# Optimization experiments

Hardware: AMD Instinct MI355X
Metric: run time of the kernel (lower is better)

## Reference

```python
import jax, jax.numpy as jnp
import numpy as np

N_NODES = 50000
N_EDGES = 800000
IN_C = 64
OUT_C = 64
HEADS = 4
N_LAYERS = 2
BN_EPS = 1e-5
NEG_SLOPE = 0.2


def setup_inputs() -> dict:
    key = jax.random.key(0)
    ks = jax.random.split(key, 20)
    inp = {
        "x": jax.random.normal(ks[0], (N_NODES, IN_C), dtype=jnp.float32),
        "edge_index": jax.random.randint(ks[1], (2, N_EDGES), 0, N_NODES, dtype=jnp.int64),
        "edge_weight": jax.random.uniform(ks[2], (N_EDGES,), dtype=jnp.float32),
    }
    # per-layer GATConv + BN params (glorot-ish init)
    for i in range(N_LAYERS):
        k = 3 + i * 5
        scale = 1.0 / np.sqrt(IN_C)
        inp[f"W{i}"] = jax.random.normal(ks[k], (IN_C, HEADS * OUT_C), dtype=jnp.float32) * scale
        inp[f"asrc{i}"] = jax.random.normal(ks[k + 1], (HEADS, OUT_C), dtype=jnp.float32) * scale
        inp[f"adst{i}"] = jax.random.normal(ks[k + 2], (HEADS, OUT_C), dtype=jnp.float32) * scale
        inp[f"b{i}"] = jnp.zeros((OUT_C,), dtype=jnp.float32)
        inp[f"gamma{i}"] = jnp.ones((OUT_C,), dtype=jnp.float32)
        inp[f"beta{i}"] = jnp.zeros((OUT_C,), dtype=jnp.float32)
    return inp


def _gat_layer(x, src, dst, W, a_src, a_dst, b):
    # x: [N, C_in]; src/dst: [E'] (with self loops). Per-head dim = OUT_C.
    xh = (x @ W).reshape(-1, HEADS, OUT_C)          # [N, H, C]
    al_src = jnp.sum(xh * a_src[None], axis=-1)      # [N, H]
    al_dst = jnp.sum(xh * a_dst[None], axis=-1)      # [N, H]
    e = jax.nn.leaky_relu(al_src[src] + al_dst[dst], NEG_SLOPE)  # [E', H]
    # segment softmax over edges sharing a destination node
    m = jax.lax.stop_gradient(jax.ops.segment_max(e, dst, num_segments=N_NODES))
    p = jnp.exp(e - m[dst])
    denom = jax.ops.segment_sum(p, dst, num_segments=N_NODES)
    alpha = p / (denom[dst] + 1e-16)                 # [E', H]
    out = jax.ops.segment_sum(alpha[:, :, None] * xh[src], dst, num_segments=N_NODES)  # [N,H,C]
    return out.mean(axis=1) + b                      # concat=False -> mean over heads


def _batchnorm(x, gamma, beta):
    mu = x.mean(axis=0)
    var = x.var(axis=0)
    return gamma * (x - mu) * jax.lax.rsqrt(var + BN_EPS) + beta


def reference(x, edge_index, edge_weight, W0, asrc0, adst0, b0, gamma0, beta0,
              W1, asrc1, adst1, b1, gamma1, beta1):
    # edge_weight is passed as edge_attr to PyG GATConv but edge_dim=None -> ignored.
    loop = jnp.arange(N_NODES, dtype=edge_index.dtype)
    src = jnp.concatenate([edge_index[0], loop])  # add_self_loops=True (PyG default)
    dst = jnp.concatenate([edge_index[1], loop])
    params = [(W0, asrc0, adst0, b0, gamma0, beta0),
              (W1, asrc1, adst1, b1, gamma1, beta1)]
    saved = None
    for (W, a_s, a_d, b, g, bt) in params:
        x = _gat_layer(x, src, dst, W, a_s, a_d, b)
        saved = x
        x = _batchnorm(x, g, bt)
        x = jax.nn.relu(x)
        # dropout(0.5) is identity in eval mode
    return (x, saved)
```

## Files before the change

kernel.cpp:

```cpp
#include <hip/hip_runtime.h>
#include <stdint.h>

#define NEG_SLOPE 0.2f
#define BN_EPS 1e-5f

typedef __attribute__((ext_vector_type(8))) short bf16x8;
typedef __attribute__((ext_vector_type(4))) float f32x4;

__device__ __forceinline__ float bf2f(unsigned short u) {
  union { unsigned int i; float f; } v; v.i = ((unsigned int)u) << 16; return v.f;
}
__device__ __forceinline__ float asf(unsigned int u) {
  union { unsigned int i; float f; } v; v.i = u; return v.f;
}
__device__ __forceinline__ unsigned short f2bf(float f) {
  union { float f; unsigned int i; } v; v.f = f;
  unsigned int i = v.i;
  return (unsigned short)((i + 0x7fffu + ((i >> 16) & 1u)) >> 16);
}
__device__ __forceinline__ float loadF(const void* p, long long i, int f32) {
  return f32 ? ((const float*)p)[i] : bf2f(((const unsigned short*)p)[i]);
}
__device__ __forceinline__ int edge_at(const void* ei, long long idx, int is64) {
  return is64 ? (int)((const long long*)ei)[idx] : ((const int*)ei)[idx];
}

__global__ void detect_kernel(const unsigned short* __restrict__ x,
                              const int* __restrict__ ei32,
                              int* __restrict__ flags) {
  __shared__ int wild, oddnz;
  if (threadIdx.x == 0) { wild = 0; oddnz = 0; }
  __syncthreads();
  int lw = 0, lo = 0;
  for (int i = threadIdx.x; i < 4096; i += 256) {
    unsigned short u = x[i];
    int ex = (u >> 7) & 0xFF;
    if (ex >= 0x86) lw++;
    if (ei32[2 * i + 1] != 0) lo++;
  }
  if (lw) atomicAdd(&wild, lw);
  if (lo) atomicAdd(&oddnz, lo);
  __syncthreads();
  if (threadIdx.x == 0) { flags[0] = (wild > 64) ? 1 : 0; flags[1] = (oddnz == 0) ? 1 : 0; }
}

__global__ __launch_bounds__(256) void wtrans_kernel(
    const void* __restrict__ W0, const void* __restrict__ as0, const void* __restrict__ ad0,
    const void* __restrict__ W1, const void* __restrict__ as1, const void* __restrict__ ad1,
    const int* __restrict__ flags,
    unsigned short* __restrict__ WTx0, unsigned short* __restrict__ WTx1) {
  const void* W = blockIdx.x ? W1 : W0;
  const void* asrc = blockIdx.x ? as1 : as0;
  const void* adst = blockIdx.x ? ad1 : ad0;
  unsigned short* WTx = blockIdx.x ? WTx1 : WTx0;
  int f32 = flags[0];
  __shared__ unsigned short Wl[64 * 258];
  int t = threadIdx.x;
  for (int i = t; i < 64 * 256; i += 256) {
    int k = i >> 8, c = i & 255;
    Wl[k * 258 + c] = f32 ? f2bf(((const float*)W)[i]) : ((const unsigned short*)W)[i];
  }
  __syncthreads();
  {
    int c = t;
    #pragma unroll
    for (int k8 = 0; k8 < 64; k8 += 8) {
      unsigned int p0 = (unsigned int)Wl[(k8 + 0) * 258 + c] | ((unsigned int)Wl[(k8 + 1) * 258 + c] << 16);
      unsigned int p1 = (unsigned int)Wl[(k8 + 2) * 258 + c] | ((unsigned int)Wl[(k8 + 3) * 258 + c] << 16);
      unsigned int p2 = (unsigned int)Wl[(k8 + 4) * 258 + c] | ((unsigned int)Wl[(k8 + 5) * 258 + c] << 16);
      unsigned int p3 = (unsigned int)Wl[(k8 + 6) * 258 + c] | ((unsigned int)Wl[(k8 + 7) * 258 + c] << 16);
      uint4 pk; pk.x = p0; pk.y = p1; pk.z = p2; pk.w = p3;
      *(uint4*)&WTx[c * 64 + k8] = pk;
    }
  }
  for (int idx = t; idx < 512; idx += 256) {
    int r = idx >> 6;
    int k = idx & 63;
    int h = r & 3;
    const void* av = (r >> 2) ? adst : asrc;
    float acc = 0.f;
    #pragma unroll 8
    for (int c = 0; c < 64; c++)
      acc += bf2f(Wl[k * 258 + h * 64 + c]) * loadF(av, h * 64 + c, f32);
    WTx[(256 + r) * 64 + k] = f2bf(acc);
  }
  for (int idx = t; idx < 512; idx += 256) WTx[264 * 64 + idx] = 0;
}

__global__ __launch_bounds__(256) void hist_kernel(const void* __restrict__ ei, int E, int N,
                                                   const int* __restrict__ flags,
                                                   int* __restrict__ deg) {
  int e = blockIdx.x * 256 + threadIdx.x;
  if (e >= E) return;
  int is64 = flags[1];
  int d = edge_at(ei, (long long)E + e, is64);
  d = (d < 0 || d >= N) ? 0 : d;
  atomicAdd(&deg[d], 1);
}

__global__ __launch_bounds__(256) void partial_kernel(const int* __restrict__ deg,
                                                      int* __restrict__ blocksum, int N) {
  int t = threadIdx.x;
  int idx = blockIdx.x * 256 + t;
  int v = (idx < N) ? deg[idx] : 0;
  #pragma unroll
  for (int o = 1; o < 64; o <<= 1) v += __shfl_xor(v, o);
  __shared__ int ws[4];
  if ((t & 63) == 0) ws[t >> 6] = v;
  __syncthreads();
  if (t == 0) blocksum[blockIdx.x] = ws[0] + ws[1] + ws[2] + ws[3];
}

__global__ void scan_base_kernel(const int* __restrict__ blocksum,
                                 int* __restrict__ blockbase, int B) {
  int lane = threadIdx.x;
  int base = 0;
  if (lane == 0) blockbase[0] = 0;
  for (int start = 0; start < B; start += 64) {
    int idx = start + lane;
    int v = (idx < B) ? blocksum[idx] : 0;
    int sc = v;
    #pragma unroll
    for (int o = 1; o < 64; o <<= 1) {
      int u = __shfl_up(sc, o);
      if (lane >= o) sc += u;
    }
    if (idx < B) blockbase[idx + 1] = base + sc;
    base = __shfl(base + sc, 63);
  }
}

__global__ __launch_bounds__(256) void scan_final_kernel(const int* __restrict__ deg,
                                                         const int* __restrict__ blockbase,
                                                         int* __restrict__ offsets, int N) {
  int t = threadIdx.x;
  int lane = t & 63;
  int wid = t >> 6;
  int idx = blockIdx.x * 256 + t;
  int v = (idx < N) ? deg[idx] : 0;
  int sc = v;
  #pragma unroll
  for (int o = 1; o < 64; o <<= 1) {
    int u = __shfl_up(sc, o);
    if (lane >= o) sc += u;
  }
  __shared__ int ws[4];
  if (lane == 63) ws[wid] = sc;
  __syncthreads();
  int add = 0;
  #pragma unroll
  for (int w = 0; w < 4; w++) if (w < wid) add += ws[w];
  if (idx < N) offsets[idx + 1] = blockbase[blockIdx.x] + add + sc;
  if (idx == 0) offsets[0] = 0;
}

__global__ __launch_bounds__(256) void scatter_kernel(
    const void* __restrict__ ei, int E, int N, const int* __restrict__ flags,
    const int* __restrict__ offsets, int* __restrict__ cursor,
    int* __restrict__ csr_src) {
  int e = blockIdx.x * 256 + threadIdx.x;
  if (e >= E) return;
  int is64 = flags[1];
  int s = edge_at(ei, e, is64);
  int d = edge_at(ei, (long long)E + e, is64);
  s = (s < 0 || s >= N) ? 0 : s;
  d = (d < 0 || d >= N) ? 0 : d;
  int pos = offsets[d] + atomicAdd(&cursor[d], 1);
  csr_src[pos] = s;
}

__global__ __launch_bounds__(256, 3) void gemm_mfma(
    const void* __restrict__ x, const unsigned short* __restrict__ WTx,
    const int* __restrict__ flags, int mode,
    const float* __restrict__ gsum, const float* __restrict__ gsq,
    const void* __restrict__ gamma, const void* __restrict__ beta,
    unsigned short* __restrict__ xh, float* __restrict__ als, float* __restrict__ ald,
    int N) {
  __shared__ unsigned short WTs[272 * 68];
  __shared__ unsigned short RP[4][16 * 68];
  __shared__ float bnsc[64], bnsh[64];
  int f32 = flags[0];
  int t = threadIdx.x;
  for (int i = t; i < 272 * 8; i += 256) {
    int c = i >> 3, g = i & 7;
    uint4 v = ((const uint4*)WTx)[i];
    *(uint4*)&WTs[c * 68 + g * 8] = v;
  }
  if (mode == 1 && t < 64) {
    float mu = gsum[t] / (float)N;
    float var = fmaxf(gsq[t] / (float)N - mu * mu, 0.f);
    float sc = loadF(gamma, t, f32) * rsqrtf(var + BN_EPS);
    bnsc[t] = sc;
    bnsh[t] = loadF(beta, t, f32) - mu * sc;
  }
  __syncthreads();

  int wave = t >> 6, lane = t & 63;
  int q = lane >> 4, r16 = lane & 15;
  unsigned short* rp = RP[wave];

  #pragma unroll
  for (int rb = 0; rb < 2; rb++) {
    int m0 = blockIdx.x * 128 + rb * 64 + wave * 16;
    if (m0 >= N) break;
    int row = m0 + r16;
    int rowc = row < N ? row : N - 1;

    bf16x8 a0, a1;
    if (mode == 1) {
      const float* xp = (const float*)x + (size_t)rowc * 64 + q * 8;
      float va[8], vb[8];
      *(float4*)&va[0] = ((const float4*)xp)[0];
      *(float4*)&va[4] = ((const float4*)xp)[1];
      *(float4*)&vb[0] = ((const float4*)(xp + 32))[0];
      *(float4*)&vb[4] = ((const float4*)(xp + 32))[1];
      int k0 = q * 8;
      #pragma unroll
      for (int jj = 0; jj < 8; jj++) {
        float v = fmaxf(va[jj] * bnsc[k0 + jj] + bnsh[k0 + jj], 0.f);
        float w = fmaxf(vb[jj] * bnsc[k0 + 32 + jj] + bnsh[k0 + 32 + jj], 0.f);
        a0[jj] = (short)f2bf(v);
        a1[jj] = (short)f2bf(w);
      }
    } else if (f32) {
      const float* xp = (const float*)x + (size_t)rowc * 64 + q * 8;
      float va[8], vb[8];
      *(float4*)&va[0] = ((const float4*)xp)[0];
      *(float4*)&va[4] = ((const float4*)xp)[1];
      *(float4*)&vb[0] = ((const float4*)(xp + 32))[0];
      *(float4*)&vb[4] = ((const float4*)(xp + 32))[1];
      #pragma unroll
      for (int jj = 0; jj < 8; jj++) {
        a0[jj] = (short)f2bf(va[jj]);
        a1[jj] = (short)f2bf(vb[jj]);
      }
    } else {
      const unsigned short* xp = (const unsigned short*)x + (size_t)rowc * 64 + q * 8;
      a0 = *(const bf16x8*)xp;
      a1 = *(const bf16x8*)(xp + 32);
    }

    f32x4 acc[17];
    #pragma unroll
    for (int tt = 0; tt < 17; tt++) acc[tt] = (f32x4){0.f, 0.f, 0.f, 0.f};
    #pragma unroll
    for (int tt = 0; tt < 17; tt++) {
      int c = tt * 16 + r16;
      bf16x8 b0 = *(const bf16x8*)&WTs[c * 68 + q * 8];
      bf16x8 b1 = *(const bf16x8*)&WTs[c * 68 + 32 + q * 8];
      acc[tt] = __builtin_amdgcn_mfma_f32_16x16x32_bf16(a0, b0, acc[tt], 0, 0, 0);
      acc[tt] = __builtin_amdgcn_mfma_f32_16x16x32_bf16(a1, b1, acc[tt], 0, 0, 0);
    }

    {
      int obase = m0 + q * 4;
      #pragma unroll
      for (int rr = 0; rr < 4; rr++) {
        int orow = obase + rr;
        if (orow < N) {
          if (r16 < 4) als[orow * 4 + r16] = acc[16][rr];
          else if (r16 < 8) ald[orow * 4 + (r16 - 4)] = acc[16][rr];
        }
      }
    }
    #pragma unroll
    for (int g4 = 0; g4 < 4; g4++) {
      #pragma unroll
      for (int tt2 = 0; tt2 < 4; tt2++) {
        int tile = g4 * 4 + tt2;
        #pragma unroll
        for (int rr = 0; rr < 4; rr++)
          rp[(q * 4 + rr) * 68 + tt2 * 16 + r16] = f2bf(acc[tile][rr]);
      }
      #pragma unroll
      for (int i = 0; i < 2; i++) {
        int g = i * 64 + lane;
        int r = g >> 3;
        int grp = g & 7;
        uint4 v = *(const uint4*)&rp[r * 68 + grp * 8];
        int orow = m0 + r;
        if (orow < N) ((uint4*)xh)[(size_t)orow * 32 + g4 * 8 + grp] = v;
      }
    }
  }
}

__global__ __launch_bounds__(256) void agg_kernel(
    const unsigned short* __restrict__ xh,
    const float* __restrict__ als, const float* __restrict__ ald,
    const int* __restrict__ offsets, const int* __restrict__ csr_src,
    const void* __restrict__ bias, const int* __restrict__ flags,
    float* __restrict__ y, int N) {
  int lane = threadIdx.x & 63;
  int wid = threadIdx.x >> 6;
  int n = blockIdx.x * 4 + wid;
  if (n >= N) return;
  int half = lane >> 5;
  int hl = lane & 31;
  int h = hl >> 3;
  const uint4* xv = (const uint4*)xh;
  float ad = ald[n * 4 + h];
  float acc0 = 0.f, acc1 = 0.f, acc2 = 0.f, acc3 = 0.f;
  float acc4 = 0.f, acc5 = 0.f, acc6 = 0.f, acc7 = 0.f;
  float dsum = 0.f;
  if (half == 0) {
    float e = als[n * 4 + h] + ad;
    e = (e > 0.f) ? e : NEG_SLOPE * e;
    float p = __expf(e);
    dsum = p;
    uint4 v = xv[(size_t)n * 32 + hl];
    acc0 = p * asf(v.x << 16); acc1 = p * asf(v.x & 0xffff0000u);
    acc2 = p * asf(v.y << 16); acc3 = p * asf(v.y & 0xffff0000u);
    acc4 = p * asf(v.z << 16); acc5 = p * asf(v.z & 0xffff0000u);
    acc6 = p * asf(v.w << 16); acc7 = p * asf(v.w & 0xffff0000u);
  }
  int beg = offsets[n], end = offsets[n + 1];
  int j = beg;
  for (; j + 8 <= end; j += 8) {
    int s0 = csr_src[j + 0 + half];
    int s1 = csr_src[j + 2 + half];
    int s2 = csr_src[j + 4 + half];
    int s3 = csr_src[j + 6 + half];
    uint4 v0 = xv[(size_t)s0 * 32 + hl];
    uint4 v1 = xv[(size_t)s1 * 32 + hl];
    uint4 v2 = xv[(size_t)s2 * 32 + hl];
    uint4 v3 = xv[(size_t)s3 * 32 + hl];
    float e0 = als[s0 * 4 + h] + ad;
    float e1 = als[s1 * 4 + h] + ad;
    float e2 = als[s2 * 4 + h] + ad;
    float e3 = als[s3 * 4 + h] + ad;
    e0 = (e0 > 0.f) ? e0 : NEG_SLOPE * e0;
    e1 = (e1 > 0.f) ? e1 : NEG_SLOPE * e1;
    e2 = (e2 > 0.f) ? e2 : NEG_SLOPE * e2;
    e3 = (e3 > 0.f) ? e3 : NEG_SLOPE * e3;
    float p0 = __expf(e0);
    float p1 = __expf(e1);
    float p2 = __expf(e2);
    float p3 = __expf(e3);
    dsum += p0 + p1 + p2 + p3;
    acc0 += p0 * asf(v0.x << 16) + p1 * asf(v1.x << 16)
          + p2 * asf(v2.x << 16) + p3 * asf(v3.x << 16);
    acc1 += p0 * asf(v0.x & 0xffff0000u) + p1 * asf(v1.x & 0xffff0000u)
          + p2 * asf(v2.x & 0xffff0000u) + p3 * asf(v3.x & 0xffff0000u);
    acc2 += p0 * asf(v0.y << 16) + p1 * asf(v1.y << 16)
          + p2 * asf(v2.y << 16) + p3 * asf(v3.y << 16);
    acc3 += p0 * asf(v0.y & 0xffff0000u) + p1 * asf(v1.y & 0xffff0000u)
          + p2 * asf(v2.y & 0xffff0000u) + p3 * asf(v3.y & 0xffff0000u);
    acc4 += p0 * asf(v0.z << 16) + p1 * asf(v1.z << 16)
          + p2 * asf(v2.z << 16) + p3 * asf(v3.z << 16);
    acc5 += p0 * asf(v0.z & 0xffff0000u) + p1 * asf(v1.z & 0xffff0000u)
          + p2 * asf(v2.z & 0xffff0000u) + p3 * asf(v3.z & 0xffff0000u);
    acc6 += p0 * asf(v0.w << 16) + p1 * asf(v1.w << 16)
          + p2 * asf(v2.w << 16) + p3 * asf(v3.w << 16);
    acc7 += p0 * asf(v0.w & 0xffff0000u) + p1 * asf(v1.w & 0xffff0000u)
          + p2 * asf(v2.w & 0xffff0000u) + p3 * asf(v3.w & 0xffff0000u);
  }
  for (; j < end; j += 2) {
    int jj = j + half;
    if (jj < end) {
      int s = csr_src[jj];
      uint4 v = xv[(size_t)s * 32 + hl];
      float e = als[s * 4 + h] + ad;
      e = (e > 0.f) ? e : NEG_SLOPE * e;
      float p = __expf(e);
      dsum += p;
      acc0 += p * asf(v.x << 16); acc1 += p * asf(v.x & 0xffff0000u);
      acc2 += p * asf(v.y << 16); acc3 += p * asf(v.y & 0xffff0000u);
      acc4 += p * asf(v.z << 16); acc5 += p * asf(v.z & 0xffff0000u);
      acc6 += p * asf(v.w << 16); acc7 += p * asf(v.w & 0xffff0000u);
    }
  }
  dsum += __shfl_xor(dsum, 32);
  acc0 += __shfl_xor(acc0, 32); acc1 += __shfl_xor(acc1, 32);
  acc2 += __shfl_xor(acc2, 32); acc3 += __shfl_xor(acc3, 32);
  acc4 += __shfl_xor(acc4, 32); acc5 += __shfl_xor(acc5, 32);
  acc6 += __shfl_xor(acc6, 32); acc7 += __shfl_xor(acc7, 32);
  float inv = 1.0f / dsum;
  acc0 *= inv; acc1 *= inv; acc2 *= inv; acc3 *= inv;
  acc4 *= inv; acc5 *= inv; acc6 *= inv; acc7 *= inv;
  acc0 += __shfl_xor(acc0, 8); acc0 += __shfl_xor(acc0, 16);
  acc1 += __shfl_xor(acc1, 8); acc1 += __shfl_xor(acc1, 16);
  acc2 += __shfl_xor(acc2, 8); acc2 += __shfl_xor(acc2, 16);
  acc3 += __shfl_xor(acc3, 8); acc3 += __shfl_xor(acc3, 16);
  acc4 += __shfl_xor(acc4, 8); acc4 += __shfl_xor(acc4, 16);
  acc5 += __shfl_xor(acc5, 8); acc5 += __shfl_xor(acc5, 16);
  acc6 += __shfl_xor(acc6, 8); acc6 += __shfl_xor(acc6, 16);
  acc7 += __shfl_xor(acc7, 8); acc7 += __shfl_xor(acc7, 16);
  if (lane < 8) {
    int f32 = flags[0];
    int cb = 8 * lane;
    float4 o0, o1;
    o0.x = 0.25f * acc0 + loadF(bias, cb + 0, f32);
    o0.y = 0.25f * acc1 + loadF(bias, cb + 1, f32);
    o0.z = 0.25f * acc2 + loadF(bias, cb + 2, f32);
    o0.w = 0.25f * acc3 + loadF(bias, cb + 3, f32);
    o1.x = 0.25f * acc4 + loadF(bias, cb + 4, f32);
    o1.y = 0.25f * acc5 + loadF(bias, cb + 5, f32);
    o1.z = 0.25f * acc6 + loadF(bias, cb + 6, f32);
    o1.w = 0.25f * acc7 + loadF(bias, cb + 7, f32);
    *(float4*)(y + (size_t)n * 64 + cb) = o0;
    *(float4*)(y + (size_t)n * 64 + cb + 4) = o1;
  }
}

__global__ __launch_bounds__(256) void stats_kernel(const float* __restrict__ y,
                                                    float* __restrict__ gsum,
                                                    float* __restrict__ gsq, int N) {
  __shared__ float ls[256], lq[256];
  int t = threadIdx.x;
  int c = t & 63;
  int r0 = blockIdx.x * 4 + (t >> 6);
  float s = 0.f, q = 0.f;
  for (int r = r0; r < N; r += gridDim.x * 4) {
    float v = y[(size_t)r * 64 + c];
    s += v; q += v * v;
  }
  ls[t] = s; lq[t] = q;
  __syncthreads();
  if (t < 64) {
    s = ls[t] + ls[t + 64] + ls[t + 128] + ls[t + 192];
    q = lq[t] + lq[t + 64] + lq[t + 128] + lq[t + 192];
    atomicAdd(&gsum[c], s);
    atomicAdd(&gsq[c], q);
  }
}

__global__ __launch_bounds__(256) void bn_kernel(
    const float* __restrict__ y, const float* __restrict__ gsum, const float* __restrict__ gsq,
    const void* __restrict__ gamma, const void* __restrict__ beta,
    const int* __restrict__ flags, float* __restrict__ out_f, int N) {
  int i = blockIdx.x * 256 + threadIdx.x;
  if (i >= N * 16) return;
  int f32 = flags[0];
  int cg = i & 15;
  float4 v = ((const float4*)y)[i];
  float4 s = ((const float4*)gsum)[cg];
  float4 q = ((const float4*)gsq)[cg];
  float inv_n = 1.0f / (float)N;
  float vv[4] = {v.x, v.y, v.z, v.w};
  float ss[4] = {s.x, s.y, s.z, s.w};
  float qq[4] = {q.x, q.y, q.z, q.w};
  float o[4];
  #pragma unroll
  for (int k = 0; k < 4; k++) {
    float g = loadF(gamma, 4 * cg + k, f32);
    float b = loadF(beta, 4 * cg + k, f32);
    float mu = ss[k] * inv_n;
    float var = fmaxf(qq[k] * inv_n - mu * mu, 0.f);
    float r = g * (vv[k] - mu) * rsqrtf(var + BN_EPS) + b;
    o[k] = r > 0.f ? r : 0.f;
  }
  float4 ov; ov.x = o[0]; ov.y = o[1]; ov.z = o[2]; ov.w = o[3];
  ((float4*)out_f)[i] = ov;
}

extern "C" void kernel_launch(void* const* d_in, const int* in_sizes, int n_in,
                              void* d_out, int out_size, void* d_ws, size_t ws_size,
                              hipStream_t stream) {
  const void* x    = d_in[0];
  const void* ei   = d_in[1];
  const void* W0    = d_in[3];
  const void* asrc0 = d_in[4];
  const void* adst0 = d_in[5];
  const void* b0    = d_in[6];
  const void* g0    = d_in[7];
  const void* be0   = d_in[8];
  const void* W1    = d_in[9];
  const void* asrc1 = d_in[10];
  const void* adst1 = d_in[11];
  const void* b1    = d_in[12];
  const void* g1    = d_in[13];
  const void* be1   = d_in[14];

  int N = in_sizes[0] / 64;
  int E = in_sizes[1] / 2;
  int NB = (N + 255) / 256;
  int NG = (N + 127) / 128;
  int NA = (N + 3) / 4;

  char* p = (char*)d_ws;
  auto alloc = [&](size_t bytes) -> char* {
    char* r = p;
    p += (bytes + 255) & ~(size_t)255;
    return r;
  };
  int* flags    = (int*)alloc(256);
  int* deg      = (int*)alloc((size_t)N * 4);
  int* cursor   = (int*)alloc((size_t)N * 4);
  int* offsets  = (int*)alloc((size_t)(N + 1) * 4);
  int* blocksum = (int*)alloc((size_t)NB * 4);
  int* blockbase= (int*)alloc((size_t)(NB + 1) * 4);
  int* csr_src  = (int*)alloc((size_t)E * 4);
  unsigned short* WTx0 = (unsigned short*)alloc(272 * 64 * 2);
  unsigned short* WTx1 = (unsigned short*)alloc(272 * 64 * 2);
  unsigned short* xh = (unsigned short*)alloc((size_t)N * 256 * 2);
  float* als    = (float*)alloc((size_t)N * 4 * 4);
  float* ald    = (float*)alloc((size_t)N * 4 * 4);
  float* y      = (float*)alloc((size_t)N * 64 * 4);
  float* gsum0  = (float*)alloc(256);
  float* gsq0   = (float*)alloc(256);
  float* gsum1  = (float*)alloc(256);
  float* gsq1   = (float*)alloc(256);

  hipMemsetAsync(deg, 0, (size_t)N * 4, stream);
  hipMemsetAsync(cursor, 0, (size_t)N * 4, stream);
  hipMemsetAsync(gsum0, 0, 1024, stream);

  detect_kernel<<<1, 256, 0, stream>>>((const unsigned short*)x, (const int*)ei, flags);
  wtrans_kernel<<<2, 256, 0, stream>>>(W0, asrc0, adst0, W1, asrc1, adst1, flags, WTx0, WTx1);

  hist_kernel<<<(E + 255) / 256, 256, 0, stream>>>(ei, E, N, flags, deg);
  partial_kernel<<<NB, 256, 0, stream>>>(deg, blocksum, N);
  scan_base_kernel<<<1, 64, 0, stream>>>(blocksum, blockbase, NB);
  scan_final_kernel<<<NB, 256, 0, stream>>>(deg, blockbase, offsets, N);
  scatter_kernel<<<(E + 255) / 256, 256, 0, stream>>>(ei, E, N, flags, offsets, cursor, csr_src);

  float* out_x = (float*)d_out;
  float* out_saved = out_x + (size_t)N * 64;

  gemm_mfma<<<NG, 256, 0, stream>>>(x, WTx0, flags, 0, (const float*)nullptr,
                                    (const float*)nullptr, nullptr, nullptr,
                                    xh, als, ald, N);
  agg_kernel<<<NA, 256, 0, stream>>>(xh, als, ald, offsets, csr_src, b0, flags, y, N);
  stats_kernel<<<250, 256, 0, stream>>>(y, gsum0, gsq0, N);
  gemm_mfma<<<NG, 256, 0, stream>>>(y, WTx1, flags, 1, gsum0, gsq0, g0, be0,
                                    xh, als, ald, N);
  agg_kernel<<<NA, 256, 0, stream>>>(xh, als, ald, offsets, csr_src, b1, flags, out_saved, N);
  stats_kernel<<<250, 256, 0, stream>>>(out_saved, gsum1, gsq1, N);
  bn_kernel<<<(N * 16 + 255) / 256, 256, 0, stream>>>(out_saved, gsum1, gsq1, g1, be1,
                                                      flags, out_x, N);
}
```

Measured before the change: 419.4 us.

## Merge detect into weight transform, single-block scan seeding cursors, bigger GEMM tiles

Folds the input-format detection into the weight transform kernel, so each block computes its own flags and one launch goes away. The three-kernel degree scan becomes a single 1024-thread block that writes the offsets and seeds the cursor array with each node's start offset. That removes the cursor memset and the offsets lookup in the scatter kernel. Each GEMM block also handles 256 rows instead of 128, which halves the grid and amortises the shared-memory weight load. The single-block scan is serial per thread and reads deg with strided, uncoalesced accesses, and the larger GEMM tiles reduce parallelism.

```diff
diff --git a/kernel.cpp b/kernel.cpp
--- a/kernel.cpp
+++ b/kernel.cpp
@@ -25,37 +25,36 @@
   return is64 ? (int)((const long long*)ei)[idx] : ((const int*)ei)[idx];
 }
 
-__global__ void detect_kernel(const unsigned short* __restrict__ x,
-                              const int* __restrict__ ei32,
-                              int* __restrict__ flags) {
-  __shared__ int wild, oddnz;
-  if (threadIdx.x == 0) { wild = 0; oddnz = 0; }
-  __syncthreads();
-  int lw = 0, lo = 0;
-  for (int i = threadIdx.x; i < 4096; i += 256) {
-    unsigned short u = x[i];
-    int ex = (u >> 7) & 0xFF;
-    if (ex >= 0x86) lw++;
-    if (ei32[2 * i + 1] != 0) lo++;
-  }
-  if (lw) atomicAdd(&wild, lw);
-  if (lo) atomicAdd(&oddnz, lo);
-  __syncthreads();
-  if (threadIdx.x == 0) { flags[0] = (wild > 64) ? 1 : 0; flags[1] = (oddnz == 0) ? 1 : 0; }
-}
-
 __global__ __launch_bounds__(256) void wtrans_kernel(
+    const unsigned short* __restrict__ x, const int* __restrict__ ei32,
     const void* __restrict__ W0, const void* __restrict__ as0, const void* __restrict__ ad0,
     const void* __restrict__ W1, const void* __restrict__ as1, const void* __restrict__ ad1,
-    const int* __restrict__ flags,
+    int* __restrict__ flags,
     unsigned short* __restrict__ WTx0, unsigned short* __restrict__ WTx1) {
+  __shared__ int wild, oddnz;
+  __shared__ unsigned short Wl[64 * 258];
+  int t = threadIdx.x;
+  if (t == 0) { wild = 0; oddnz = 0; }
+  __syncthreads();
+  {
+    int lw = 0, lo = 0;
+    for (int i = t; i < 4096; i += 256) {
+      unsigned short u = x[i];
+      int ex = (u >> 7) & 0xFF;
+      if (ex >= 0x86) lw++;
+      if (ei32[2 * i + 1] != 0) lo++;
+    }
+    if (lw) atomicAdd(&wild, lw);
+    if (lo) atomicAdd(&oddnz, lo);
+  }
+  __syncthreads();
+  int f32 = (wild > 64) ? 1 : 0;
+  if (blockIdx.x == 0 && t == 0) { flags[0] = f32; flags[1] = (oddnz == 0) ? 1 : 0; }
+
   const void* W = blockIdx.x ? W1 : W0;
   const void* asrc = blockIdx.x ? as1 : as0;
   const void* adst = blockIdx.x ? ad1 : ad0;
   unsigned short* WTx = blockIdx.x ? WTx1 : WTx0;
-  int f32 = flags[0];
-  __shared__ unsigned short Wl[64 * 258];
-  int t = threadIdx.x;
   for (int i = t; i < 64 * 256; i += 256) {
     int k = i >> 8, c = i & 255;
     Wl[k * 258 + c] = f32 ? f2bf(((const float*)W)[i]) : ((const unsigned short*)W)[i];
@@ -98,66 +97,47 @@
   atomicAdd(&deg[d], 1);
 }
 
-__global__ __launch_bounds__(256) void partial_kernel(const int* __restrict__ deg,
-                                                      int* __restrict__ blocksum, int N) {
-  int t = threadIdx.x;
-  int idx = blockIdx.x * 256 + t;
-  int v = (idx < N) ? deg[idx] : 0;
-  #pragma unroll
-  for (int o = 1; o < 64; o <<= 1) v += __shfl_xor(v, o);
-  __shared__ int ws[4];
-  if ((t & 63) == 0) ws[t >> 6] = v;
-  __syncthreads();
-  if (t == 0) blocksum[blockIdx.x] = ws[0] + ws[1] + ws[2] + ws[3];
-}
-
-__global__ void scan_base_kernel(const int* __restrict__ blocksum,
-                                 int* __restrict__ blockbase, int B) {
-  int lane = threadIdx.x;
-  int base = 0;
-  if (lane == 0) blockbase[0] = 0;
-  for (int start = 0; start < B; start += 64) {
-    int idx = start + lane;
-    int v = (idx < B) ? blocksum[idx] : 0;
-    int sc = v;
-    #pragma unroll
-    for (int o = 1; o < 64; o <<= 1) {
-      int u = __shfl_up(sc, o);
-      if (lane >= o) sc += u;
-    }
-    if (idx < B) blockbase[idx + 1] = base + sc;
-    base = __shfl(base + sc, 63);
-  }
-}
-
-__global__ __launch_bounds__(256) void scan_final_kernel(const int* __restrict__ deg,
-                                                         const int* __restrict__ blockbase,
-                                                         int* __restrict__ offsets, int N) {
+__global__ __launch_bounds__(1024) void scan_kernel(const int* __restrict__ deg,
+                                                    int* __restrict__ offsets,
+                                                    int* __restrict__ cursor, int N) {
+  __shared__ int wsum[16];
   int t = threadIdx.x;
   int lane = t & 63;
   int wid = t >> 6;
-  int idx = blockIdx.x * 256 + t;
-  int v = (idx < N) ? deg[idx] : 0;
-  int sc = v;
+  int C = (N + 1023) / 1024;
+  int b0 = t * C;
+  int s = 0;
+  for (int i = 0; i < C; i++) {
+    int idx = b0 + i;
+    if (idx < N) s += deg[idx];
+  }
+  int sc = s;
   #pragma unroll
   for (int o = 1; o < 64; o <<= 1) {
     int u = __shfl_up(sc, o);
     if (lane >= o) sc += u;
   }
-  __shared__ int ws[4];
-  if (lane == 63) ws[wid] = sc;
+  if (lane == 63) wsum[wid] = sc;
   __syncthreads();
-  int add = 0;
+  int wbase = 0;
   #pragma unroll
-  for (int w = 0; w < 4; w++) if (w < wid) add += ws[w];
-  if (idx < N) offsets[idx + 1] = blockbase[blockIdx.x] + add + sc;
-  if (idx == 0) offsets[0] = 0;
+  for (int w = 0; w < 16; w++) if (w < wid) wbase += wsum[w];
+  int base = wbase + sc - s;
+  if (t == 0) offsets[0] = 0;
+  int run = base;
+  for (int i = 0; i < C; i++) {
+    int idx = b0 + i;
+    if (idx < N) {
+      cursor[idx] = run;
+      run += deg[idx];
+      offsets[idx + 1] = run;
+    }
+  }
 }
 
 __global__ __launch_bounds__(256) void scatter_kernel(
     const void* __restrict__ ei, int E, int N, const int* __restrict__ flags,
-    const int* __restrict__ offsets, int* __restrict__ cursor,
-    int* __restrict__ csr_src) {
+    int* __restrict__ cursor, int* __restrict__ csr_src) {
   int e = blockIdx.x * 256 + threadIdx.x;
   if (e >= E) return;
   int is64 = flags[1];
@@ -165,7 +145,7 @@
   int d = edge_at(ei, (long long)E + e, is64);
   s = (s < 0 || s >= N) ? 0 : s;
   d = (d < 0 || d >= N) ? 0 : d;
-  int pos = offsets[d] + atomicAdd(&cursor[d], 1);
+  int pos = atomicAdd(&cursor[d], 1);
   csr_src[pos] = s;
 }
 
@@ -199,9 +179,8 @@
   int q = lane >> 4, r16 = lane & 15;
   unsigned short* rp = RP[wave];
 
-  #pragma unroll
-  for (int rb = 0; rb < 2; rb++) {
-    int m0 = blockIdx.x * 128 + rb * 64 + wave * 16;
+  for (int rb = 0; rb < 4; rb++) {
+    int m0 = blockIdx.x * 256 + rb * 64 + wave * 16;
     if (m0 >= N) break;
     int row = m0 + r16;
     int rowc = row < N ? row : N - 1;
@@ -474,8 +453,7 @@
 
   int N = in_sizes[0] / 64;
   int E = in_sizes[1] / 2;
-  int NB = (N + 255) / 256;
-  int NG = (N + 127) / 128;
+  int NG = (N + 255) / 256;
   int NA = (N + 3) / 4;
 
   char* p = (char*)d_ws;
@@ -488,8 +466,6 @@
   int* deg      = (int*)alloc((size_t)N * 4);
   int* cursor   = (int*)alloc((size_t)N * 4);
   int* offsets  = (int*)alloc((size_t)(N + 1) * 4);
-  int* blocksum = (int*)alloc((size_t)NB * 4);
-  int* blockbase= (int*)alloc((size_t)(NB + 1) * 4);
   int* csr_src  = (int*)alloc((size_t)E * 4);
   unsigned short* WTx0 = (unsigned short*)alloc(272 * 64 * 2);
   unsigned short* WTx1 = (unsigned short*)alloc(272 * 64 * 2);
@@ -503,17 +479,14 @@
   float* gsq1   = (float*)alloc(256);
 
   hipMemsetAsync(deg, 0, (size_t)N * 4, stream);
-  hipMemsetAsync(cursor, 0, (size_t)N * 4, stream);
   hipMemsetAsync(gsum0, 0, 1024, stream);
 
-  detect_kernel<<<1, 256, 0, stream>>>((const unsigned short*)x, (const int*)ei, flags);
-  wtrans_kernel<<<2, 256, 0, stream>>>(W0, asrc0, adst0, W1, asrc1, adst1, flags, WTx0, WTx1);
+  wtrans_kernel<<<2, 256, 0, stream>>>((const unsigned short*)x, (const int*)ei,
+                                       W0, asrc0, adst0, W1, asrc1, adst1, flags, WTx0, WTx1);
 
   hist_kernel<<<(E + 255) / 256, 256, 0, stream>>>(ei, E, N, flags, deg);
-  partial_kernel<<<NB, 256, 0, stream>>>(deg, blocksum, N);
-  scan_base_kernel<<<1, 64, 0, stream>>>(blocksum, blockbase, NB);
-  scan_final_kernel<<<NB, 256, 0, stream>>>(deg, blockbase, offsets, N);
-  scatter_kernel<<<(E + 255) / 256, 256, 0, stream>>>(ei, E, N, flags, offsets, cursor, csr_src);
+  scan_kernel<<<1, 1024, 0, stream>>>(deg, offsets, cursor, N);
+  scatter_kernel<<<(E + 255) / 256, 256, 0, stream>>>(ei, E, N, flags, cursor, csr_src);
 
   float* out_x = (float*)d_out;
   float* out_saved = out_x + (size_t)N * 64;
```

Measured after the change: 549.6 us. 31.0% more time.
